# Performance work log

Measured on AMD Instinct MI355X. Metric: run time of the kernel, lower is better.

Reference implementation:

```python
import jax, jax.numpy as jnp
import numpy as np

X_DIM, Y_DIM, HIDDEN, N = 768, 768, 300, 768


def setup_inputs() -> dict:
    key = jax.random.key(0)
    ks = jax.random.split(key, 7)
    lim1 = 1.0 / np.sqrt(X_DIM + Y_DIM)
    lim2 = 1.0 / np.sqrt(HIDDEN)
    return {
        "x_samples": jax.random.normal(ks[0], (N, X_DIM), dtype=jnp.float32),
        "y_samples": jax.random.normal(ks[1], (N, Y_DIM), dtype=jnp.float32),
        "perm": jax.random.permutation(ks[2], N).astype(jnp.int32),
        # Linear 1: (x_dim+y_dim) -> hidden, torch default uniform init
        "W1": jax.random.uniform(ks[3], (HIDDEN, X_DIM + Y_DIM), jnp.float32, -lim1, lim1),
        "b1": jax.random.uniform(ks[4], (HIDDEN,), jnp.float32, -lim1, lim1),
        # Linear 2: hidden -> 1
        "W2": jax.random.uniform(ks[5], (1, HIDDEN), jnp.float32, -lim2, lim2),
        "b2": jax.random.uniform(ks[6], (1,), jnp.float32, -lim2, lim2),
    }


def reference(x_samples, y_samples, perm, W1, b1, W2, b2):
    n = x_samples.shape[0]
    x_dim = x_samples.shape[1]
    # First linear is separable across the concat: split W1 into x- and y-parts.
    hx = x_samples @ W1[:, :x_dim].T            # [N, H]
    hy = y_samples @ W1[:, x_dim:].T            # [N, H]
    w2 = W2[0]                                   # [H]
    # T0: matched pairs (x_i, y_i)
    t0 = jax.nn.softplus(jax.nn.relu(hx + hy + b1) @ w2 + b2[0])   # [N]
    # T1[i, j] = F(x_j, y_perm[i]) -- pairwise tile, [N, N, H] intermediate
    hyp = hy[perm]                               # [N, H]
    hpair = jax.nn.relu(hyp[:, None, :] + hx[None, :, :] + b1)     # [N, N, H]
    t1 = jax.nn.softplus(hpair @ w2 + b2[0])     # [N, N]
    lower_bound = t0.mean() - (jax.nn.logsumexp(t1, axis=1).mean() - jnp.log(n).astype(t1.dtype))
    return lower_bound
```

## Files before the change

### kernel.cpp

```cpp
#include <hip/hip_runtime.h>
#include <math.h>

#define NN   768
#define HH   300
#define KD   768

#define P_OFF    0
#define PKS_STR  245760
#define PG_STR   1966080
#define CF_OFF   3932160
#define AF_OFF   4177920
#define SP_OFF   4423680
#define SP_STR   589824
#define ES_OFF   9142272
#define T0_OFF   9143040

__global__ __launch_bounds__(256) void k1_gemm(
    const float* __restrict__ x, const float* __restrict__ y,
    const int* __restrict__ perm, const float* __restrict__ W1,
    float* __restrict__ wsf)
{
    const int tid = threadIdx.x;
    const int tx = tid & 15;
    const int ty = tid >> 4;
    const int i0 = blockIdx.x * 128;
    const int h0 = blockIdx.y * 64;
    const int g  = blockIdx.z & 1;
    const int ks = blockIdx.z >> 1;
    const int kbeg = ks * 96;

    const float* src = g ? y : x;
    const int koff = g ? KD : 0;

    __shared__ float Xt[32][132];
    __shared__ float Wt[32][68];

    float4 acc[4][2];
    #pragma unroll
    for (int r = 0; r < 4; ++r) { acc[r][0] = make_float4(0,0,0,0);
                                  acc[r][1] = make_float4(0,0,0,0); }

    const int kq = (tid & 7) << 2;
    const float* xp[4];
    int xr[4];
    #pragma unroll
    for (int it = 0; it < 4; ++it) {
        int row = ((tid + it*256) >> 3);
        int gr = i0 + row;
        if (g) gr = perm[gr];
        xp[it] = src + (size_t)gr * KD + kbeg + kq;
        xr[it] = row;
    }
    const float* wp[2];
    int wr[2]; bool wv[2];
    #pragma unroll
    for (int it = 0; it < 2; ++it) {
        int hrow = ((tid + it*256) >> 3);
        int hg = h0 + hrow;
        wv[it] = hg < HH;
        wp[it] = W1 + (size_t)(wv[it] ? hg : 0) * (2*KD) + koff + kbeg + kq;
        wr[it] = hrow;
    }

    for (int kb = 0; kb < 96; kb += 32) {
        float4 xv[4], wvv[2];
        #pragma unroll
        for (int it = 0; it < 4; ++it) xv[it] = *(const float4*)(xp[it] + kb);
        #pragma unroll
        for (int it = 0; it < 2; ++it) {
            wvv[it] = *(const float4*)(wp[it] + kb);
            if (!wv[it]) wvv[it] = make_float4(0,0,0,0);
        }
        if (kb) __syncthreads();
        #pragma unroll
        for (int it = 0; it < 4; ++it) {
            Xt[kq+0][xr[it]] = xv[it].x; Xt[kq+1][xr[it]] = xv[it].y;
            Xt[kq+2][xr[it]] = xv[it].z; Xt[kq+3][xr[it]] = xv[it].w;
        }
        #pragma unroll
        for (int it = 0; it < 2; ++it) {
            Wt[kq+0][wr[it]] = wvv[it].x; Wt[kq+1][wr[it]] = wvv[it].y;
            Wt[kq+2][wr[it]] = wvv[it].z; Wt[kq+3][wr[it]] = wvv[it].w;
        }
        __syncthreads();

        #pragma unroll 8
        for (int k = 0; k < 32; ++k) {
            float4 a  = *(const float4*)&Wt[k][4*ty];
            float4 b0 = *(const float4*)&Xt[k][4*tx];
            float4 b1v = *(const float4*)&Xt[k][64 + 4*tx];
            float ar[4] = {a.x, a.y, a.z, a.w};
            #pragma unroll
            for (int r = 0; r < 4; ++r) {
                acc[r][0].x = fmaf(ar[r], b0.x,  acc[r][0].x);
                acc[r][0].y = fmaf(ar[r], b0.y,  acc[r][0].y);
                acc[r][0].z = fmaf(ar[r], b0.z,  acc[r][0].z);
                acc[r][0].w = fmaf(ar[r], b0.w,  acc[r][0].w);
                acc[r][1].x = fmaf(ar[r], b1v.x, acc[r][1].x);
                acc[r][1].y = fmaf(ar[r], b1v.y, acc[r][1].y);
                acc[r][1].z = fmaf(ar[r], b1v.z, acc[r][1].z);
                acc[r][1].w = fmaf(ar[r], b1v.w, acc[r][1].w);
            }
        }
    }

    float* dst = wsf + P_OFF + (size_t)(g*8 + ks) * PKS_STR;
    #pragma unroll
    for (int r = 0; r < 4; ++r) {
        float* rp = dst + (size_t)(h0 + 4*ty + r) * NN + i0;
        *(float4*)(rp + 4*tx)      = acc[r][0];
        *(float4*)(rp + 64 + 4*tx) = acc[r][1];
    }
}

__global__ __launch_bounds__(256) void k1b_combine(
    const float* __restrict__ b1, float* __restrict__ wsf)
{
    int idx = blockIdx.x * 256 + threadIdx.x;
    int g = idx >= 61440;
    int rem = idx - g * 61440;
    int h = rem / 192;
    int i4 = (rem % 192) * 4;

    float4 o = make_float4(0.f,0.f,0.f,0.f);
    if (h < HH) {
        const float* p = wsf + P_OFF + (size_t)g * PG_STR + (size_t)h * NN + i4;
        #pragma unroll
        for (int ks = 0; ks < 8; ++ks) {
            float4 v = *(const float4*)(p + (size_t)ks * PKS_STR);
            o.x += v.x; o.y += v.y; o.z += v.z; o.w += v.w;
        }
        if (g) {
            float bv = b1[h];
            o.x += bv; o.y += bv; o.z += bv; o.w += bv;
        }
    }
    float* dst = wsf + (g ? AF_OFF : CF_OFF) + (size_t)h * NN + i4;
    *(float4*)dst = o;
}

__global__ __launch_bounds__(256) void k2_pair(
    const float* __restrict__ wsf, const float* __restrict__ w2,
    float* __restrict__ sp)
{
    const int tid = threadIdx.x;
    const int tx = tid & 15;
    const int ty = tid >> 4;
    const int j0 = blockIdx.x * 96;
    const int i0 = blockIdx.y * 96;
    const int p  = blockIdx.z;
    const int h0 = p * 38;

    const float* AF = wsf + AF_OFF;
    const float* CF = wsf + CF_OFF;

    __shared__ float As[38][100];
    __shared__ float Cs[38][100];
    __shared__ float w2s[38];

    for (int e = tid; e < 912; e += 256) {
        int h = e / 24, q = (e % 24) * 4;
        *(float4*)&As[h][q] = *(const float4*)(AF + (size_t)(h0 + h) * NN + i0 + q);
    }
    for (int e = tid; e < 912; e += 256) {
        int h = e / 24, q = (e % 24) * 4;
        *(float4*)&Cs[h][q] = *(const float4*)(CF + (size_t)(h0 + h) * NN + j0 + q);
    }
    if (tid < 38) {
        int h = h0 + tid;
        w2s[tid] = (h < HH) ? w2[h] : 0.f;
    }
    __syncthreads();

    float acc[6][6];
    #pragma unroll
    for (int r = 0; r < 6; ++r)
        #pragma unroll
        for (int c = 0; c < 6; ++c) acc[r][c] = 0.f;

    #pragma unroll 2
    for (int h = 0; h < 38; ++h) {
        float wh = w2s[h];
        float4 a03 = *(const float4*)&As[h][4*ty];
        float2 a45 = *(const float2*)&As[h][64 + 2*ty];
        float4 c03 = *(const float4*)&Cs[h][4*tx];
        float2 c45 = *(const float2*)&Cs[h][64 + 2*tx];
        float ar[6] = {a03.x, a03.y, a03.z, a03.w, a45.x, a45.y};
        float cr[6] = {c03.x, c03.y, c03.z, c03.w, c45.x, c45.y};
        #pragma unroll
        for (int r = 0; r < 6; ++r) {
            #pragma unroll
            for (int c = 0; c < 6; ++c) {
                float t = fmaxf(ar[r] + cr[c], 0.f);
                acc[r][c] = fmaf(t, wh, acc[r][c]);
            }
        }
    }

    float* dst = sp + (size_t)p * SP_STR;
    #pragma unroll
    for (int r = 0; r < 6; ++r) {
        int i = (r < 4) ? (i0 + 4*ty + r) : (i0 + 64 + 2*ty + (r - 4));
        float* rp = dst + (size_t)i * NN + j0;
        *(float4*)(rp + 4*tx) =
            make_float4(acc[r][0], acc[r][1], acc[r][2], acc[r][3]);
        *(float2*)(rp + 64 + 2*tx) = make_float2(acc[r][4], acc[r][5]);
    }
}

__global__ __launch_bounds__(256) void k2e_rows(
    const float* __restrict__ wsf, const int* __restrict__ perm,
    const float* __restrict__ b2,
    float* __restrict__ esum, float* __restrict__ t0c)
{
    const int tid = threadIdx.x;
    const float b2v = b2[0];
    const int row = blockIdx.x;
    const int pj = perm[row];
    const float* spr = wsf + SP_OFF + (size_t)row * NN;
    __shared__ float red[256];

    float e = 0.f;
    #pragma unroll
    for (int jj = 0; jj < 3; ++jj) {
        int j = tid + jj * 256;
        float s = 0.f;
        #pragma unroll
        for (int p = 0; p < 8; ++p) s += spr[(size_t)p * SP_STR + j];
        float u = s + b2v;
        e += expf(u);
        if (j == pj) {
            t0c[row] = (u > 0.f) ? u + log1pf(expf(-u)) : log1pf(expf(u));
        }
    }
    red[tid] = e;
    __syncthreads();
    for (int s = 128; s > 0; s >>= 1) {
        if (tid < s) red[tid] += red[tid + s];
        __syncthreads();
    }
    if (tid == 0) esum[row] = red[0];
}

__global__ __launch_bounds__(256) void k3_final(
    const float* __restrict__ wsf, float* __restrict__ out)
{
    const int tid = threadIdx.x;
    const float* esum = wsf + ES_OFF;
    const float* t0   = wsf + T0_OFF;

    double st0 = 0.0, slse = 0.0;
    for (int i = tid; i < NN; i += 256) {
        st0  += (double)t0[i];
        slse += log((double)NN + (double)esum[i]);
    }
    __shared__ double sa[256], sb[256];
    sa[tid] = st0; sb[tid] = slse;
    __syncthreads();
    for (int s = 128; s > 0; s >>= 1) {
        if (tid < s) { sa[tid] += sa[tid+s]; sb[tid] += sb[tid+s]; }
        __syncthreads();
    }
    if (tid == 0) {
        double lb = sa[0]/(double)NN - (sb[0]/(double)NN - log((double)NN));
        out[0] = (float)lb;
    }
}

extern "C" void kernel_launch(void* const* d_in, const int* in_sizes, int n_in,
                              void* d_out, int out_size, void* d_ws, size_t ws_size,
                              hipStream_t stream) {
    const float* x    = (const float*)d_in[0];
    const float* y    = (const float*)d_in[1];
    const int*   perm = (const int*)  d_in[2];
    const float* W1   = (const float*)d_in[3];
    const float* b1   = (const float*)d_in[4];
    const float* W2   = (const float*)d_in[5];
    const float* b2   = (const float*)d_in[6];
    float* wsf = (float*)d_ws;
    float* out = (float*)d_out;

    k1_gemm    <<<dim3(6,5,16), 256, 0, stream>>>(x, y, perm, W1, wsf);
    k1b_combine<<<480,          256, 0, stream>>>(b1, wsf);
    k2_pair    <<<dim3(8,8,8),  256, 0, stream>>>(wsf, W2, wsf + SP_OFF);
    k2e_rows   <<<NN,           256, 0, stream>>>(wsf, perm, b2,
                                                  wsf + ES_OFF, wsf + T0_OFF);
    k3_final   <<<1,            256, 0, stream>>>(wsf, out);
}
```

Baseline: 118.5 us.

## Fuse pairwise hidden reduction with row exp-sum and drop split-H partials

The pairwise kernel now loops over the full hidden dimension in 50-wide chunks, using register double-buffering to prefetch the next chunk from global memory while computing the current one. This removes the 8-way split over H. Exp, softplus and the per-row partial exp-sums are computed inside the pairwise kernel, so the separate row kernel and the 8×N×N partial-sum buffer go away. The tile shrinks to 48×48 with 3×3 outputs per thread, giving 256 blocks. That cuts a lot of global traffic, but each thread reuses fewer loaded values and the grid offers less parallelism.

```diff
diff --git a/kernel.cpp b/kernel.cpp
--- a/kernel.cpp
+++ b/kernel.cpp
@@ -10,10 +10,8 @@
 #define PG_STR   1966080
 #define CF_OFF   3932160
 #define AF_OFF   4177920
-#define SP_OFF   4423680
-#define SP_STR   589824
-#define ES_OFF   9142272
-#define T0_OFF   9143040
+#define RS_OFF   4423680
+#define T0_OFF   4435968
 
 __global__ __launch_bounds__(256) void k1_gemm(
     const float* __restrict__ x, const float* __restrict__ y,
@@ -141,118 +139,114 @@
 
 __global__ __launch_bounds__(256) void k2_pair(
     const float* __restrict__ wsf, const float* __restrict__ w2,
-    float* __restrict__ sp)
+    const int* __restrict__ perm, const float* __restrict__ b2,
+    float* __restrict__ rsO, float* __restrict__ t0c)
 {
     const int tid = threadIdx.x;
     const int tx = tid & 15;
     const int ty = tid >> 4;
-    const int j0 = blockIdx.x * 96;
-    const int i0 = blockIdx.y * 96;
-    const int p  = blockIdx.z;
-    const int h0 = p * 38;
+    const int j0 = blockIdx.x * 48;
+    const int i0 = blockIdx.y * 48;
 
     const float* AF = wsf + AF_OFF;
     const float* CF = wsf + CF_OFF;
 
-    __shared__ float As[38][100];
-    __shared__ float Cs[38][100];
-    __shared__ float w2s[38];
-
-    for (int e = tid; e < 912; e += 256) {
-        int h = e / 24, q = (e % 24) * 4;
-        *(float4*)&As[h][q] = *(const float4*)(AF + (size_t)(h0 + h) * NN + i0 + q);
-    }
-    for (int e = tid; e < 912; e += 256) {
-        int h = e / 24, q = (e % 24) * 4;
-        *(float4*)&Cs[h][q] = *(const float4*)(CF + (size_t)(h0 + h) * NN + j0 + q);
-    }
-    if (tid < 38) {
-        int h = h0 + tid;
-        w2s[tid] = (h < HH) ? w2[h] : 0.f;
-    }
-    __syncthreads();
-
-    float acc[6][6];
-    #pragma unroll
-    for (int r = 0; r < 6; ++r)
-        #pragma unroll
-        for (int c = 0; c < 6; ++c) acc[r][c] = 0.f;
-
-    #pragma unroll 2
-    for (int h = 0; h < 38; ++h) {
-        float wh = w2s[h];
-        float4 a03 = *(const float4*)&As[h][4*ty];
-        float2 a45 = *(const float2*)&As[h][64 + 2*ty];
-        float4 c03 = *(const float4*)&Cs[h][4*tx];
-        float2 c45 = *(const float2*)&Cs[h][64 + 2*tx];
-        float ar[6] = {a03.x, a03.y, a03.z, a03.w, a45.x, a45.y};
-        float cr[6] = {c03.x, c03.y, c03.z, c03.w, c45.x, c45.y};
-        #pragma unroll
-        for (int r = 0; r < 6; ++r) {
+    __shared__ float As[50][48];
+    __shared__ float Cs[50][48];
+    __shared__ float w2s[50];
+
+    int ho[3], qo[3]; bool val[3];
+    #pragma unroll
+    for (int s = 0; s < 3; ++s) {
+        int e = tid + s * 256;
+        val[s] = e < 600;
+        ho[s] = e / 12;
+        qo[s] = (e % 12) * 4;
+    }
+
+    float acc[3][3];
+    #pragma unroll
+    for (int r = 0; r < 3; ++r)
+        #pragma unroll
+        for (int c = 0; c < 3; ++c) acc[r][c] = 0.f;
+
+    float4 pa[3] = {}, pc[3] = {};
+    #pragma unroll
+    for (int s = 0; s < 3; ++s) if (val[s]) {
+        pa[s] = *(const float4*)(AF + (size_t)ho[s] * NN + i0 + qo[s]);
+        pc[s] = *(const float4*)(CF + (size_t)ho[s] * NN + j0 + qo[s]);
+    }
+    float pw = (tid < 50) ? w2[tid] : 0.f;
+
+    for (int cc = 0; cc < 6; ++cc) {
+        if (cc) __syncthreads();
+        #pragma unroll
+        for (int s = 0; s < 3; ++s) if (val[s]) {
+            *(float4*)&As[ho[s]][qo[s]] = pa[s];
+            *(float4*)&Cs[ho[s]][qo[s]] = pc[s];
+        }
+        if (tid < 50) w2s[tid] = pw;
+        __syncthreads();
+
+        if (cc < 5) {
+            const float* a = AF + (size_t)(cc + 1) * 50 * NN;
+            const float* c = CF + (size_t)(cc + 1) * 50 * NN;
             #pragma unroll
-            for (int c = 0; c < 6; ++c) {
-                float t = fmaxf(ar[r] + cr[c], 0.f);
-                acc[r][c] = fmaf(t, wh, acc[r][c]);
+            for (int s = 0; s < 3; ++s) if (val[s]) {
+                pa[s] = *(const float4*)(a + (size_t)ho[s] * NN + i0 + qo[s]);
+                pc[s] = *(const float4*)(c + (size_t)ho[s] * NN + j0 + qo[s]);
             }
-        }
-    }
-
-    float* dst = sp + (size_t)p * SP_STR;
-    #pragma unroll
-    for (int r = 0; r < 6; ++r) {
-        int i = (r < 4) ? (i0 + 4*ty + r) : (i0 + 64 + 2*ty + (r - 4));
-        float* rp = dst + (size_t)i * NN + j0;
-        *(float4*)(rp + 4*tx) =
-            make_float4(acc[r][0], acc[r][1], acc[r][2], acc[r][3]);
-        *(float2*)(rp + 64 + 2*tx) = make_float2(acc[r][4], acc[r][5]);
-    }
-}
-
-__global__ __launch_bounds__(256) void k2e_rows(
-    const float* __restrict__ wsf, const int* __restrict__ perm,
-    const float* __restrict__ b2,
-    float* __restrict__ esum, float* __restrict__ t0c)
-{
-    const int tid = threadIdx.x;
+            if (tid < 50) pw = w2[(cc + 1) * 50 + tid];
+        }
+
+        #pragma unroll 5
+        for (int h = 0; h < 50; ++h) {
+            float wh = w2s[h];
+            float ar[3] = {As[h][ty], As[h][ty + 16], As[h][ty + 32]};
+            float cr[3] = {Cs[h][tx], Cs[h][tx + 16], Cs[h][tx + 32]};
+            #pragma unroll
+            for (int r = 0; r < 3; ++r)
+                #pragma unroll
+                for (int c = 0; c < 3; ++c)
+                    acc[r][c] = fmaf(fmaxf(ar[r] + cr[c], 0.f), wh, acc[r][c]);
+        }
+    }
+
     const float b2v = b2[0];
-    const int row = blockIdx.x;
-    const int pj = perm[row];
-    const float* spr = wsf + SP_OFF + (size_t)row * NN;
-    __shared__ float red[256];
-
-    float e = 0.f;
-    #pragma unroll
-    for (int jj = 0; jj < 3; ++jj) {
-        int j = tid + jj * 256;
-        float s = 0.f;
-        #pragma unroll
-        for (int p = 0; p < 8; ++p) s += spr[(size_t)p * SP_STR + j];
-        float u = s + b2v;
-        e += expf(u);
-        if (j == pj) {
-            t0c[row] = (u > 0.f) ? u + log1pf(expf(-u)) : log1pf(expf(u));
-        }
-    }
-    red[tid] = e;
-    __syncthreads();
-    for (int s = 128; s > 0; s >>= 1) {
-        if (tid < s) red[tid] += red[tid + s];
-        __syncthreads();
-    }
-    if (tid == 0) esum[row] = red[0];
+    #pragma unroll
+    for (int r = 0; r < 3; ++r) {
+        int i = i0 + ty + 16 * r;
+        int pj = perm[i];
+        float rsum = 0.f;
+        #pragma unroll
+        for (int c = 0; c < 3; ++c) {
+            int j = j0 + tx + 16 * c;
+            float u = acc[r][c] + b2v;
+            rsum += expf(u);
+            if (j == pj)
+                t0c[i] = (u > 0.f) ? u + log1pf(expf(-u)) : log1pf(expf(u));
+        }
+        #pragma unroll
+        for (int off = 8; off; off >>= 1)
+            rsum += __shfl_xor(rsum, off, 16);
+        if (tx == 0) rsO[(size_t)blockIdx.x * NN + i] = rsum;
+    }
 }
 
 __global__ __launch_bounds__(256) void k3_final(
     const float* __restrict__ wsf, float* __restrict__ out)
 {
     const int tid = threadIdx.x;
-    const float* esum = wsf + ES_OFF;
-    const float* t0   = wsf + T0_OFF;
+    const float* rs = wsf + RS_OFF;
+    const float* t0 = wsf + T0_OFF;
 
     double st0 = 0.0, slse = 0.0;
     for (int i = tid; i < NN; i += 256) {
+        float s = 0.f;
+        #pragma unroll
+        for (int jb = 0; jb < 16; ++jb) s += rs[(size_t)jb * NN + i];
         st0  += (double)t0[i];
-        slse += log((double)NN + (double)esum[i]);
+        slse += log((double)NN + (double)s);
     }
     __shared__ double sa[256], sb[256];
     sa[tid] = st0; sb[tid] = slse;
@@ -282,8 +276,7 @@
 
     k1_gemm    <<<dim3(6,5,16), 256, 0, stream>>>(x, y, perm, W1, wsf);
     k1b_combine<<<480,          256, 0, stream>>>(b1, wsf);
-    k2_pair    <<<dim3(8,8,8),  256, 0, stream>>>(wsf, W2, wsf + SP_OFF);
-    k2e_rows   <<<NN,           256, 0, stream>>>(wsf, perm, b2,
-                                                  wsf + ES_OFF, wsf + T0_OFF);
+    k2_pair    <<<dim3(16,16),  256, 0, stream>>>(wsf, W2, perm, b2,
+                                                  wsf + RS_OFF, wsf + T0_OFF);
     k3_final   <<<1,            256, 0, stream>>>(wsf, out);
 }
```

Result: slower. 129.1 us (+8.9%).
